# Optimization experiments

Measured on AMD Instinct MI355X. Metric: run time of the kernel, lower is better.

## Reference

```python
import math
import jax, jax.numpy as jnp
import numpy as np

B, T, D, K = 16, 2048, 1024, 8  # batch, seq, neurons, clusters (GELU5_K_MAX)


def setup_inputs() -> dict:
    key = jax.random.key(0)
    k1, k2, k3 = jax.random.split(key, 3)
    x = jax.random.normal(k1, (B, T, D), dtype=jnp.float32)
    mus = jax.random.normal(k2, (K, D), dtype=jnp.float32)          # cluster means (buffer)
    ws = jax.nn.softmax(jax.random.normal(k3, (K,)))                 # normalized mixture weights (buffer)
    log_tau = jnp.full((D,), math.log(2.0), dtype=jnp.float32)       # GELU2_TEMP = 2.0
    log_blend = jnp.full((D,), math.log(0.3 / 0.7), dtype=jnp.float32)  # logit(GELU2_BLEND=0.3)
    return {"x": x, "mus": mus, "ws": ws, "log_tau": log_tau, "log_blend": log_blend}


def _gelu_tanh(y):
    c = math.sqrt(2.0 / math.pi)
    return 0.5 * y * (1.0 + jnp.tanh(c * (y + 0.044715 * y * y * y)))


def reference(x, mus, ws, log_tau, log_blend):
    tau = jnp.exp(log_tau)              # (D,) suppression sharpness > 0
    alpha = jax.nn.sigmoid(log_blend)   # (D,) max suppression depth in (0,1)

    # Responsibilities computed under no_grad in torch -> stop_gradient here.
    x_mean = jax.lax.stop_gradient(jnp.mean(x, axis=(0, 1)))  # (D,)
    mus_c = jax.lax.stop_gradient(mus)
    ws_c = jax.lax.stop_gradient(ws)
    dist = jnp.sqrt(jnp.mean((x_mean[None, :] - mus_c) ** 2, axis=-1))  # (K,) RMS distances
    r = jax.nn.softmax(jnp.log(ws_c) - dist)                            # (K,)

    # famil_i = sum_k r_k * exp(-tau_i * |x_i - mu_k_i|), accumulated over K
    # to avoid materializing a (B,T,K,D) intermediate.
    def body(acc, mu_r):
        mu, rk = mu_r
        return acc + rk * jnp.exp(-tau * jnp.abs(x - mu)), None

    famil, _ = jax.lax.scan(body, jnp.zeros_like(x), (mus_c, r))  # (B,T,D)

    y = x * (1.0 - alpha * famil)
    return _gelu_tanh(y)
```

## Files before the change

### kernel.cpp

```cpp
#include <hip/hip_runtime.h>
#include <math.h>

#define BT    32768
#define DD    1024
#define DV    256
#define KC    8
#define NPART 512
#define G3    1024
#define RPB3  32

typedef float fv4 __attribute__((ext_vector_type(4)));

__global__ __launch_bounds__(256) void kA_partial(const float* __restrict__ x,
                                                  float* __restrict__ part,
                                                  int rows_per_blk) {
    const int tid = threadIdx.x;
    const fv4* xv = (const fv4*)x;
    const long row0 = (long)blockIdx.x * rows_per_blk;
    fv4 acc = (fv4)(0.f);

    for (int r = 0; r < rows_per_blk; r += 8) {
        fv4 v[8];
#pragma unroll
        for (int i = 0; i < 8; ++i)
            v[i] = xv[(row0 + r + i) * DV + tid];
#pragma unroll
        for (int i = 0; i < 8; ++i) acc += v[i];
    }

    ((fv4*)part)[(long)blockIdx.x * DV + tid] = acc;
}

__global__ __launch_bounds__(256) void kB_fold(const float* __restrict__ part,
                                               float* __restrict__ colsum) {
    const int tid = threadIdx.x;
    const int b = blockIdx.x;
    __shared__ fv4 red[256];

    fv4 a = ((const fv4*)part)[(long)tid * DV + b] +
            ((const fv4*)part)[(long)(tid + 256) * DV + b];
    red[tid] = a;
    __syncthreads();
#pragma unroll
    for (int s = 128; s > 0; s >>= 1) {
        if (tid < s) red[tid] += red[tid + s];
        __syncthreads();
    }
    if (tid == 0) ((fv4*)colsum)[b] = red[0];
}

__global__ __launch_bounds__(256) void kC_main(const float* __restrict__ x,
                                               const float* __restrict__ mus,
                                               const float* __restrict__ wmix,
                                               const float* __restrict__ log_tau,
                                               const float* __restrict__ log_blend,
                                               const float* __restrict__ colsum,
                                               float* __restrict__ out) {
    const int tid = threadIdx.x;
    const long row0 = (long)blockIdx.x * RPB3;
    const fv4* xv = (const fv4*)x;

    float mu[KC][4];
#pragma unroll
    for (int k = 0; k < KC; ++k) {
        fv4 m4 = ((const fv4*)mus)[k * DV + tid];
        mu[k][0] = m4.x; mu[k][1] = m4.y; mu[k][2] = m4.z; mu[k][3] = m4.w;
    }

    float rk[KC];
    {
        const float inv_bt = 1.0f / (float)BT;
        fv4 s = ((const fv4*)colsum)[tid];
        float m[4] = { s.x * inv_bt, s.y * inv_bt, s.z * inv_bt, s.w * inv_bt };
        float prt[KC];
#pragma unroll
        for (int k = 0; k < KC; ++k) {
            float d0 = m[0] - mu[k][0], d1 = m[1] - mu[k][1];
            float d2 = m[2] - mu[k][2], d3 = m[3] - mu[k][3];
            prt[k] = d0 * d0 + d1 * d1 + d2 * d2 + d3 * d3;
        }
        __shared__ float l2[KC][4];
        const int lane = tid & 63, wv = tid >> 6;
#pragma unroll
        for (int k = 0; k < KC; ++k) {
            float v = prt[k];
#pragma unroll
            for (int off = 32; off > 0; off >>= 1) v += __shfl_down(v, off, 64);
            if (lane == 0) l2[k][wv] = v;
        }
        __syncthreads();
        float logits[KC], mx = -1e30f;
#pragma unroll
        for (int k = 0; k < KC; ++k) {
            float tot = l2[k][0] + l2[k][1] + l2[k][2] + l2[k][3];
            float dist = sqrtf(tot * (1.0f / (float)DD));
            logits[k] = logf(wmix[k]) - dist;
            mx = fmaxf(mx, logits[k]);
        }
        float se = 0.f, e[KC];
#pragma unroll
        for (int k = 0; k < KC; ++k) { e[k] = expf(logits[k] - mx); se += e[k]; }
        float is = 1.f / se;
#pragma unroll
        for (int k = 0; k < KC; ++k) rk[k] = e[k] * is;
    }

    const float LOG2E = 1.44269504f;
    fv4 lt = ((const fv4*)log_tau)[tid];
    fv4 lb = ((const fv4*)log_blend)[tid];
    float tl[4], al[4];
    tl[0] = __builtin_amdgcn_exp2f(lt.x * LOG2E) * LOG2E;
    tl[1] = __builtin_amdgcn_exp2f(lt.y * LOG2E) * LOG2E;
    tl[2] = __builtin_amdgcn_exp2f(lt.z * LOG2E) * LOG2E;
    tl[3] = __builtin_amdgcn_exp2f(lt.w * LOG2E) * LOG2E;
    al[0] = 1.f / (1.f + __builtin_amdgcn_exp2f(-lb.x * LOG2E));
    al[1] = 1.f / (1.f + __builtin_amdgcn_exp2f(-lb.y * LOG2E));
    al[2] = 1.f / (1.f + __builtin_amdgcn_exp2f(-lb.z * LOG2E));
    al[3] = 1.f / (1.f + __builtin_amdgcn_exp2f(-lb.w * LOG2E));

    fv4* ov = (fv4*)out;
    for (int rr = 0; rr < RPB3; rr += 8) {
        fv4 v[8];
#pragma unroll
        for (int i = 0; i < 8; ++i)
            v[i] = xv[(row0 + rr + i) * DV + tid];
#pragma unroll
        for (int i = 0; i < 8; ++i) {
            float xin[4] = { v[i].x, v[i].y, v[i].z, v[i].w };
            float o[4];
#pragma unroll
            for (int e = 0; e < 4; ++e) {
                float xe = xin[e];
                float fam = 0.f;
#pragma unroll
                for (int k = 0; k < KC; ++k)
                    fam += rk[k] * __builtin_amdgcn_exp2f(-tl[e] * fabsf(xe - mu[k][e]));
                float y = xe * (1.f - al[e] * fam);
                float z = 0.79788456f * (y + 0.044715f * y * y * y);
                float e2 = __builtin_amdgcn_exp2f(2.88539008f * z);
                float th = 1.f - 2.f * __builtin_amdgcn_rcpf(e2 + 1.f);
                o[e] = 0.5f * y * (1.f + th);
            }
            fv4 res; res.x = o[0]; res.y = o[1]; res.z = o[2]; res.w = o[3];
            __builtin_nontemporal_store(res, &ov[(row0 + rr + i) * DV + tid]);
        }
    }
}

extern "C" void kernel_launch(void* const* d_in, const int* in_sizes, int n_in,
                              void* d_out, int out_size, void* d_ws, size_t ws_size,
                              hipStream_t stream) {
    const float* x         = (const float*)d_in[0];
    const float* mus       = (const float*)d_in[1];
    const float* wmix      = (const float*)d_in[2];
    const float* log_tau   = (const float*)d_in[3];
    const float* log_blend = (const float*)d_in[4];
    float* out = (float*)d_out;

    float* part   = (float*)d_ws;
    float* colsum = part + (long)NPART * DD;

    kA_partial<<<NPART, 256, 0, stream>>>(x, part, BT / NPART);
    kB_fold<<<DV, 256, 0, stream>>>(part, colsum);
    kC_main<<<G3, 256, 0, stream>>>(x, mus, wmix, log_tau, log_blend,
                                    colsum, out);
}
```

Measured before the change: 83.88 us.

## Fuse column-mean reduction and main pass into one cooperative kernel

Replaces the three-kernel sequence with a single cooperative kernel. Each block sums its own 32 rows, a grid sync follows, the first 256 blocks fold the partials, a second grid sync follows, and every block then computes responsibilities and processes the same rows it summed. Because each block reads its rows twice, the second read can be served from cache rather than DRAM, and two kernel launches go away. The cost is two grid-wide barriers and a residency requirement (4 blocks per CU, 1024 blocks); if the occupancy query fails that requirement, the old path runs with retuned rows per block.

```diff
diff --git a/kernel.cpp b/kernel.cpp
--- a/kernel.cpp
+++ b/kernel.cpp
@@ -1,15 +1,157 @@
 #include <hip/hip_runtime.h>
+#include <hip/hip_cooperative_groups.h>
 #include <math.h>
 
-#define BT    32768
-#define DD    1024
-#define DV    256
-#define KC    8
-#define NPART 512
-#define G3    1024
-#define RPB3  32
+namespace cg = cooperative_groups;
+
+#define BT     32768
+#define DD     1024
+#define DV     256
+#define KC     8
+#define NBLKF  1024
+#define RPBF   32
+#define NPART  512
+#define G3     2048
+#define RPB3   16
 
 typedef float fv4 __attribute__((ext_vector_type(4)));
+
+__global__ __launch_bounds__(256, 4) void fused(
+        const float* __restrict__ x,
+        const float* __restrict__ mus,
+        const float* __restrict__ wmix,
+        const float* __restrict__ log_tau,
+        const float* __restrict__ log_blend,
+        float* __restrict__ out,
+        float* __restrict__ part,
+        float* __restrict__ colsum) {
+    const int tid = threadIdx.x;
+    const int bid = blockIdx.x;
+    cg::grid_group grid = cg::this_grid();
+
+    const fv4* xv = (const fv4*)x;
+    const long row0 = (long)bid * RPBF;
+
+    __shared__ fv4 red[256];
+    __shared__ float l2[KC][4];
+
+    {
+        fv4 acc = (fv4)(0.f);
+        for (int r = 0; r < RPBF; r += 8) {
+            fv4 v[8];
+#pragma unroll
+            for (int i = 0; i < 8; ++i)
+                v[i] = xv[(row0 + r + i) * DV + tid];
+#pragma unroll
+            for (int i = 0; i < 8; ++i) acc += v[i];
+        }
+        ((fv4*)part)[(long)bid * DV + tid] = acc;
+    }
+    grid.sync();
+
+    if (bid < DV) {
+        fv4 a = (fv4)(0.f);
+#pragma unroll
+        for (int j = 0; j < NBLKF / 256; ++j)
+            a += ((const fv4*)part)[(long)(tid + j * 256) * DV + bid];
+        red[tid] = a;
+        __syncthreads();
+#pragma unroll
+        for (int s = 128; s > 0; s >>= 1) {
+            if (tid < s) red[tid] += red[tid + s];
+            __syncthreads();
+        }
+        if (tid == 0) ((fv4*)colsum)[bid] = red[0];
+    }
+    grid.sync();
+
+    float mu[KC][4];
+#pragma unroll
+    for (int k = 0; k < KC; ++k) {
+        fv4 m4 = ((const fv4*)mus)[k * DV + tid];
+        mu[k][0] = m4.x; mu[k][1] = m4.y; mu[k][2] = m4.z; mu[k][3] = m4.w;
+    }
+
+    float rk[KC];
+    {
+        const float inv_bt = 1.0f / (float)BT;
+        fv4 s = ((const fv4*)colsum)[tid];
+        float m[4] = { s.x * inv_bt, s.y * inv_bt, s.z * inv_bt, s.w * inv_bt };
+        float prt[KC];
+#pragma unroll
+        for (int k = 0; k < KC; ++k) {
+            float d0 = m[0] - mu[k][0], d1 = m[1] - mu[k][1];
+            float d2 = m[2] - mu[k][2], d3 = m[3] - mu[k][3];
+            prt[k] = d0 * d0 + d1 * d1 + d2 * d2 + d3 * d3;
+        }
+        const int lane = tid & 63, wv = tid >> 6;
+#pragma unroll
+        for (int k = 0; k < KC; ++k) {
+            float v = prt[k];
+#pragma unroll
+            for (int off = 32; off > 0; off >>= 1) v += __shfl_down(v, off, 64);
+            if (lane == 0) l2[k][wv] = v;
+        }
+        __syncthreads();
+        float logits[KC], mx = -1e30f;
+#pragma unroll
+        for (int k = 0; k < KC; ++k) {
+            float tot = l2[k][0] + l2[k][1] + l2[k][2] + l2[k][3];
+            float dist = sqrtf(tot * (1.0f / (float)DD));
+            logits[k] = logf(wmix[k]) - dist;
+            mx = fmaxf(mx, logits[k]);
+        }
+        float se = 0.f, e[KC];
+#pragma unroll
+        for (int k = 0; k < KC; ++k) { e[k] = expf(logits[k] - mx); se += e[k]; }
+        float is = 1.f / se;
+#pragma unroll
+        for (int k = 0; k < KC; ++k) rk[k] = e[k] * is;
+    }
+
+    {
+        const float LOG2E = 1.44269504f;
+        fv4 lt = ((const fv4*)log_tau)[tid];
+        fv4 lb = ((const fv4*)log_blend)[tid];
+        float tl[4], al[4];
+        tl[0] = __builtin_amdgcn_exp2f(lt.x * LOG2E) * LOG2E;
+        tl[1] = __builtin_amdgcn_exp2f(lt.y * LOG2E) * LOG2E;
+        tl[2] = __builtin_amdgcn_exp2f(lt.z * LOG2E) * LOG2E;
+        tl[3] = __builtin_amdgcn_exp2f(lt.w * LOG2E) * LOG2E;
+        al[0] = 1.f / (1.f + __builtin_amdgcn_exp2f(-lb.x * LOG2E));
+        al[1] = 1.f / (1.f + __builtin_amdgcn_exp2f(-lb.y * LOG2E));
+        al[2] = 1.f / (1.f + __builtin_amdgcn_exp2f(-lb.z * LOG2E));
+        al[3] = 1.f / (1.f + __builtin_amdgcn_exp2f(-lb.w * LOG2E));
+
+        fv4* ov = (fv4*)out;
+        for (int rr = 0; rr < RPBF; rr += 8) {
+            fv4 v[8];
+#pragma unroll
+            for (int i = 0; i < 8; ++i)
+                v[i] = xv[(row0 + rr + i) * DV + tid];
+#pragma unroll
+            for (int i = 0; i < 8; ++i) {
+                float xin[4] = { v[i].x, v[i].y, v[i].z, v[i].w };
+                float o[4];
+#pragma unroll
+                for (int e = 0; e < 4; ++e) {
+                    float xe = xin[e];
+                    float fam = 0.f;
+#pragma unroll
+                    for (int k = 0; k < KC; ++k)
+                        fam += rk[k] * __builtin_amdgcn_exp2f(-tl[e] * fabsf(xe - mu[k][e]));
+                    float y = xe * (1.f - al[e] * fam);
+                    float z = 0.79788456f * (y + 0.044715f * y * y * y);
+                    float e2 = __builtin_amdgcn_exp2f(2.88539008f * z);
+                    float th = 1.f - 2.f * __builtin_amdgcn_rcpf(e2 + 1.f);
+                    o[e] = 0.5f * y * (1.f + th);
+                }
+                fv4 res; res.x = o[0]; res.y = o[1]; res.z = o[2]; res.w = o[3];
+                __builtin_nontemporal_store(res, &ov[(row0 + rr + i) * DV + tid]);
+            }
+        }
+    }
+}
 
 __global__ __launch_bounds__(256) void kA_partial(const float* __restrict__ x,
                                                   float* __restrict__ part,
@@ -18,7 +160,6 @@
     const fv4* xv = (const fv4*)x;
     const long row0 = (long)blockIdx.x * rows_per_blk;
     fv4 acc = (fv4)(0.f);
-
     for (int r = 0; r < rows_per_blk; r += 8) {
         fv4 v[8];
 #pragma unroll
@@ -27,7 +168,6 @@
 #pragma unroll
         for (int i = 0; i < 8; ++i) acc += v[i];
     }
-
     ((fv4*)part)[(long)blockIdx.x * DV + tid] = acc;
 }
 
@@ -36,7 +176,6 @@
     const int tid = threadIdx.x;
     const int b = blockIdx.x;
     __shared__ fv4 red[256];
-
     fv4 a = ((const fv4*)part)[(long)tid * DV + b] +
             ((const fv4*)part)[(long)(tid + 256) * DV + b];
     red[tid] = a;
@@ -60,13 +199,6 @@
     const long row0 = (long)blockIdx.x * RPB3;
     const fv4* xv = (const fv4*)x;
 
-    float mu[KC][4];
-#pragma unroll
-    for (int k = 0; k < KC; ++k) {
-        fv4 m4 = ((const fv4*)mus)[k * DV + tid];
-        mu[k][0] = m4.x; mu[k][1] = m4.y; mu[k][2] = m4.z; mu[k][3] = m4.w;
-    }
-
     float rk[KC];
     {
         const float inv_bt = 1.0f / (float)BT;
@@ -75,8 +207,9 @@
         float prt[KC];
 #pragma unroll
         for (int k = 0; k < KC; ++k) {
-            float d0 = m[0] - mu[k][0], d1 = m[1] - mu[k][1];
-            float d2 = m[2] - mu[k][2], d3 = m[3] - mu[k][3];
+            fv4 mu = ((const fv4*)mus)[k * DV + tid];
+            float d0 = m[0] - mu.x, d1 = m[1] - mu.y;
+            float d2 = m[2] - mu.z, d3 = m[3] - mu.w;
             prt[k] = d0 * d0 + d1 * d1 + d2 * d2 + d3 * d3;
         }
         __shared__ float l2[KC][4];
@@ -118,14 +251,21 @@
     al[2] = 1.f / (1.f + __builtin_amdgcn_exp2f(-lb.z * LOG2E));
     al[3] = 1.f / (1.f + __builtin_amdgcn_exp2f(-lb.w * LOG2E));
 
+    float mu[KC][4];
+#pragma unroll
+    for (int k = 0; k < KC; ++k) {
+        fv4 m4 = ((const fv4*)mus)[k * DV + tid];
+        mu[k][0] = m4.x; mu[k][1] = m4.y; mu[k][2] = m4.z; mu[k][3] = m4.w;
+    }
+
     fv4* ov = (fv4*)out;
-    for (int rr = 0; rr < RPB3; rr += 8) {
-        fv4 v[8];
-#pragma unroll
-        for (int i = 0; i < 8; ++i)
+    for (int rr = 0; rr < RPB3; rr += 4) {
+        fv4 v[4];
+#pragma unroll
+        for (int i = 0; i < 4; ++i)
             v[i] = xv[(row0 + rr + i) * DV + tid];
 #pragma unroll
-        for (int i = 0; i < 8; ++i) {
+        for (int i = 0; i < 4; ++i) {
             float xin[4] = { v[i].x, v[i].y, v[i].z, v[i].w };
             float o[4];
 #pragma unroll
@@ -157,11 +297,25 @@
     const float* log_blend = (const float*)d_in[4];
     float* out = (float*)d_out;
 
-    float* part   = (float*)d_ws;
-    float* colsum = part + (long)NPART * DD;
-
-    kA_partial<<<NPART, 256, 0, stream>>>(x, part, BT / NPART);
-    kB_fold<<<DV, 256, 0, stream>>>(part, colsum);
-    kC_main<<<G3, 256, 0, stream>>>(x, mus, wmix, log_tau, log_blend,
-                                    colsum, out);
-}
+    int blocksPerCU = 0;
+    hipError_t qerr = hipOccupancyMaxActiveBlocksPerMultiprocessor(
+        &blocksPerCU, (const void*)fused, 256, 0);
+    const bool coop_ok = (qerr == hipSuccess) && (blocksPerCU * 256 >= NBLKF);
+
+    if (coop_ok) {
+        float* part   = (float*)d_ws;
+        float* colsum = part + (long)NBLKF * DD;
+        void* args[] = { (void*)&x, (void*)&mus, (void*)&wmix, (void*)&log_tau,
+                         (void*)&log_blend, (void*)&out, (void*)&part,
+                         (void*)&colsum };
+        (void)hipLaunchCooperativeKernel((const void*)fused, dim3(NBLKF),
+                                         dim3(256), args, 0, stream);
+    } else {
+        float* part   = (float*)d_ws;
+        float* colsum = part + (long)NPART * DD;
+        kA_partial<<<NPART, 256, 0, stream>>>(x, part, BT / NPART);
+        kB_fold<<<DV, 256, 0, stream>>>(part, colsum);
+        kC_main<<<G3, 256, 0, stream>>>(x, mus, wmix, log_tau, log_blend,
+                                        colsum, out);
+    }
+}
```

Measured after the change: 83.43 us. About the same (-0.5%).
